# Performance work log

Hardware: AMD Instinct MI355X
Metric: run time of the kernel (lower is better)

Reference implementation:

```python
import jax, jax.numpy as jnp
import numpy as np

B, T, NIV, H = 2048, 64, 10, 128
DT = 0.01


def _uniform(key, shape, fan_in, dtype=jnp.float32):
    bound = 1.0 / np.sqrt(fan_in)
    return jax.random.uniform(key, shape, minval=-bound, maxval=bound, dtype=dtype)


def setup_inputs() -> dict:
    key = jax.random.key(0)
    ks = jax.random.split(key, 12)
    eye = jnp.array([1.0, 0.0, 0.0, 1.0, 0.0, 1.0], dtype=jnp.float32)
    eps = jax.random.normal(ks[0], (B, T, 6), dtype=jnp.float32) * 0.1 + eye
    # free-energy MLP: layers [6+NIV, H, H, 1] (torch Linear init, stored as [in,out])
    wW1 = _uniform(ks[1], (6 + NIV, H), 6 + NIV)
    wb1 = _uniform(ks[2], (H,), 6 + NIV)
    wW2 = _uniform(ks[3], (H, H), H)
    wb2 = _uniform(ks[4], (H,), H)
    wW3 = _uniform(ks[5], (H, 1), H)
    wb3 = _uniform(ks[6], (1,), H)
    # dissipation MLP: layers [NIV, H, H, 1]; last layer is ConvexLayer (weight squared, no bias)
    dW1 = _uniform(ks[7], (NIV, H), NIV)
    db1 = _uniform(ks[8], (H,), NIV)
    dW2 = _uniform(ks[9], (H, H), H)
    db2 = _uniform(ks[10], (H,), H)
    dWc = _uniform(ks[11], (H, 1), H)
    return {"eps": eps, "wW1": wW1, "wb1": wb1, "wW2": wW2, "wb2": wb2,
            "wW3": wW3, "wb3": wb3, "dW1": dW1, "db1": db1, "dW2": dW2,
            "db2": db2, "dWc": dWc}


def reference(eps, wW1, wb1, wW2, wb2, wW3, wb3, dW1, db1, dW2, db2, dWc):
    dtype = eps.dtype
    eye = jnp.array([1.0, 0.0, 0.0, 1.0, 0.0, 1.0], dtype=dtype)
    relu2 = lambda x: jnp.square(jax.nn.relu(x))  # ReLUSquared

    def free_energy(e, xi):
        # e: [B,6], xi: [B,NIV] -> scalar potential per sample [B,1]
        x = jnp.concatenate([e - eye, xi], axis=-1)
        x = relu2(x @ wW1 + wb1)
        x = relu2(x @ wW2 + wb2)
        return x @ wW3 + wb3

    def dissipation(d):
        # d: [B,NIV] -> [B,1]; final ConvexLayer uses squared weights, no bias
        x = relu2(d @ dW1 + db1)
        x = relu2(x @ dW2 + db2)
        return x @ jnp.square(dWc)

    # grad of summed scalar potential == per-sample grads (as in torch.autograd.grad)
    grad_W = jax.grad(lambda e, xi: free_energy(e, xi).sum(), argnums=(0, 1))
    grad_D = jax.grad(lambda d: dissipation(d).sum())

    def step(xi, e_t):
        stress, df = grad_W(e_t, xi)          # dW/deps, dW/dxi
        increment = grad_D(-df)               # dD*/dd evaluated at d = -df
        return xi + DT * increment, stress

    xi0 = jnp.zeros((eps.shape[0], dW1.shape[0]), dtype=dtype)
    _, shat = jax.lax.scan(step, xi0, jnp.swapaxes(eps, 0, 1))  # scan over time
    return jnp.swapaxes(shat, 0, 1)  # [B, T, 6]
```

## Files before the change

### kernel.cpp

```cpp
#include <hip/hip_runtime.h>
#include <hip/hip_bf16.h>


#define NIV 10
#define DT_C 0.01f

__device__ __forceinline__ float bcast(float v, int l) {
    return __int_as_float(__builtin_amdgcn_readlane(__float_as_int(v), l));
}

__global__ __launch_bounds__(512, 2) void cm_kernel(
    const float* __restrict__ eps,
    const float* __restrict__ gwW1, const float* __restrict__ gwb1,
    const float* __restrict__ gwW2, const float* __restrict__ gwb2,
    const float* __restrict__ gwW3,
    const float* __restrict__ gdW1, const float* __restrict__ gdb1,
    const float* __restrict__ gdW2, const float* __restrict__ gdb2,
    const float* __restrict__ gdWc,
    float* __restrict__ out)
{
    __shared__ __align__(16) float sW2[16384];
    __shared__ __align__(16) float sD2[16384];
    __shared__ __align__(16) float sW1[2048];
    __shared__ __align__(16) float sW1T[2048];
    __shared__ __align__(16) float sD1[1280];
    __shared__ __align__(16) float sD1T[1536];
    __shared__ float sb1[128], sb2[128], sW3[128], sdb1[128], sdb2[128], sDc2[128];

    const int tid = threadIdx.x;

    for (int i = tid; i < 16384; i += 512) {
        int r = i >> 7, c = i & 127;
        int idx = (r << 7) + ((((c >> 1) ^ (r >> 1)) & 63) << 1) + (c & 1);
        sW2[idx] = gwW2[i];
        sD2[idx] = gdW2[i];
    }
    for (int i = tid; i < 2048; i += 512) {
        sW1[i] = gwW1[i];
        int k = i >> 7, r = i & 127;
        sW1T[r * 16 + k] = gwW1[i];
    }
    for (int i = tid; i < 1280; i += 512) sD1[i] = gdW1[i];
    for (int i = tid; i < 1536; i += 512) {
        int r = i / 12, m = i - r * 12;
        sD1T[i] = (m < 10) ? gdW1[m * 128 + r] : 0.f;
    }
    if (tid < 128) {
        sb1[tid]  = gwb1[tid];
        sb2[tid]  = gwb2[tid];
        sW3[tid]  = gwW3[tid];
        sdb1[tid] = gdb1[tid];
        sdb2[tid] = gdb2[tid];
        float w = gdWc[tid];
        sDc2[tid] = w * w;
    }
    __syncthreads();

    const int lane = tid & 63;
    const int wv   = tid >> 6;
    const int b    = blockIdx.x * 8 + wv;
    const int c0   = lane * 2, c1 = lane * 2 + 1;
    const int k16  = lane & 15;
    const int k12  = (k16 < 12) ? k16 : 0;

    float xi[NIV];
#pragma unroll
    for (int m = 0; m < NIV; ++m) xi[m] = 0.f;

    const float* ep = eps + b * (64 * 6);
    float*       op = out + b * (64 * 6);

    for (int t = 0; t < 64; ++t) {
        float x0[16];
        x0[0] = ep[t*6+0] - 1.f; x0[1] = ep[t*6+1];       x0[2] = ep[t*6+2];
        x0[3] = ep[t*6+3] - 1.f; x0[4] = ep[t*6+4];       x0[5] = ep[t*6+5] - 1.f;
#pragma unroll
        for (int m = 0; m < NIV; ++m) x0[6+m] = xi[m];

        float z1a = sb1[c0], z1b = sb1[c1];
#pragma unroll
        for (int k = 0; k < 16; ++k) {
            z1a = fmaf(x0[k], sW1[k*128 + c0], z1a);
            z1b = fmaf(x0[k], sW1[k*128 + c1], z1b);
        }
        float r1a = fmaxf(z1a, 0.f), r1b = fmaxf(z1b, 0.f);
        float a1a = r1a * r1a,       a1b = r1b * r1b;

        float z2a = sb2[c0], z2b = sb2[c1];
#pragma unroll 16
        for (int j = 0; j < 64; ++j) {
            float v0 = bcast(a1a, j), v1 = bcast(a1b, j);
            int o = (lane ^ j) << 1;
            const float2 w0 = *(const float2*)(sW2 + (j << 8) + o);
            const float2 w1 = *(const float2*)(sW2 + (j << 8) + 128 + o);
            z2a = fmaf(v0, w0.x, z2a); z2a = fmaf(v1, w1.x, z2a);
            z2b = fmaf(v0, w0.y, z2b); z2b = fmaf(v1, w1.y, z2b);
        }
        float r2a = fmaxf(z2a, 0.f), r2b = fmaxf(z2b, 0.f);
        float gza = 2.f * r2a * sW3[c0], gzb = 2.f * r2b * sW3[c1];

        float g1a = 0.f, g1b = 0.f;
#pragma unroll 16
        for (int j = 0; j < 64; ++j) {
            float v0 = bcast(gza, j), v1 = bcast(gzb, j);
            int o = (lane ^ j) << 1;
            const float2 wa = *(const float2*)(sW2 + c0*128 + o);
            const float2 wb = *(const float2*)(sW2 + c1*128 + o);
            g1a = fmaf(wa.x, v0, g1a); g1a = fmaf(wa.y, v1, g1a);
            g1b = fmaf(wb.x, v0, g1b); g1b = fmaf(wb.y, v1, g1b);
        }
        float gz1a = 2.f * g1a * r1a, gz1b = 2.f * g1b * r1b;

        float gx = 0.f;
#pragma unroll 16
        for (int j = 0; j < 64; ++j) {
            float v0 = bcast(gz1a, j), v1 = bcast(gz1b, j);
            gx = fmaf(v0, sW1T[(j << 5) + k16],      gx);
            gx = fmaf(v1, sW1T[(j << 5) + 16 + k16], gx);
        }
        if (lane < 6) op[t*6 + lane] = gx;

        float dm[NIV];
#pragma unroll
        for (int m = 0; m < NIV; ++m) dm[m] = -bcast(gx, 6 + m);

        float u1a = sdb1[c0], u1b = sdb1[c1];
#pragma unroll
        for (int m = 0; m < NIV; ++m) {
            u1a = fmaf(dm[m], sD1[m*128 + c0], u1a);
            u1b = fmaf(dm[m], sD1[m*128 + c1], u1b);
        }
        float p1a = fmaxf(u1a, 0.f), p1b = fmaxf(u1b, 0.f);
        float q1a = p1a * p1a,       q1b = p1b * p1b;

        float u2a = sdb2[c0], u2b = sdb2[c1];
#pragma unroll 16
        for (int j = 0; j < 64; ++j) {
            float v0 = bcast(q1a, j), v1 = bcast(q1b, j);
            int o = (lane ^ j) << 1;
            const float2 w0 = *(const float2*)(sD2 + (j << 8) + o);
            const float2 w1 = *(const float2*)(sD2 + (j << 8) + 128 + o);
            u2a = fmaf(v0, w0.x, u2a); u2a = fmaf(v1, w1.x, u2a);
            u2b = fmaf(v0, w0.y, u2b); u2b = fmaf(v1, w1.y, u2b);
        }
        float hu2a = 2.f * fmaxf(u2a, 0.f) * sDc2[c0];
        float hu2b = 2.f * fmaxf(u2b, 0.f) * sDc2[c1];

        float h1a = 0.f, h1b = 0.f;
#pragma unroll 16
        for (int j = 0; j < 64; ++j) {
            float v0 = bcast(hu2a, j), v1 = bcast(hu2b, j);
            int o = (lane ^ j) << 1;
            const float2 wa = *(const float2*)(sD2 + c0*128 + o);
            const float2 wb = *(const float2*)(sD2 + c1*128 + o);
            h1a = fmaf(wa.x, v0, h1a); h1a = fmaf(wa.y, v1, h1a);
            h1b = fmaf(wb.x, v0, h1b); h1b = fmaf(wb.y, v1, h1b);
        }
        float hu1a = 2.f * h1a * p1a, hu1b = 2.f * h1b * p1b;

        float gd = 0.f;
#pragma unroll 16
        for (int j = 0; j < 64; ++j) {
            float v0 = bcast(hu1a, j), v1 = bcast(hu1b, j);
            gd = fmaf(v0, sD1T[j*24 + k12],      gd);
            gd = fmaf(v1, sD1T[j*24 + 12 + k12], gd);
        }

#pragma unroll
        for (int m = 0; m < NIV; ++m) xi[m] = fmaf(DT_C, bcast(gd, m), xi[m]);
    }
}

extern "C" void kernel_launch(void* const* d_in, const int* in_sizes, int n_in,
                              void* d_out, int out_size, void* d_ws, size_t ws_size,
                              hipStream_t stream) {
    const float* eps = (const float*)d_in[0];
    const float* wW1 = (const float*)d_in[1];
    const float* wb1 = (const float*)d_in[2];
    const float* wW2 = (const float*)d_in[3];
    const float* wb2 = (const float*)d_in[4];
    const float* wW3 = (const float*)d_in[5];
    const float* dW1 = (const float*)d_in[7];
    const float* db1 = (const float*)d_in[8];
    const float* dW2 = (const float*)d_in[9];
    const float* db2 = (const float*)d_in[10];
    const float* dWc = (const float*)d_in[11];
    float* out = (float*)d_out;

    cm_kernel<<<dim3(256), dim3(512), 0, stream>>>(
        eps, wW1, wb1, wW2, wb2, wW3, dW1, db1, dW2, db2, dWc, out);
}
```

Before: 1.005 ms.

## Rewrite recurrent MLP step on MFMA with split fp16 hi/lo precision

Result: slower. 1.501 ms (+49.4%).

```diff
diff --git a/kernel.cpp b/kernel.cpp
--- a/kernel.cpp
+++ b/kernel.cpp
@@ -2,191 +2,401 @@
 #include <hip/hip_bf16.h>
 
 
-#define NIV 10
+typedef _Float16 h8 __attribute__((ext_vector_type(8)));
+typedef _Float16 h4 __attribute__((ext_vector_type(4)));
+typedef float    f4 __attribute__((ext_vector_type(4)));
+
+#define MFMA16(a,b,c) __builtin_amdgcn_mfma_f32_16x16x32_f16((a),(b),(c),0,0,0)
+#define LBAR() asm volatile("s_waitcnt lgkmcnt(0)" ::: "memory")
 #define DT_C 0.01f
 
-__device__ __forceinline__ float bcast(float v, int l) {
-    return __int_as_float(__builtin_amdgcn_readlane(__float_as_int(v), l));
-}
-
-__global__ __launch_bounds__(512, 2) void cm_kernel(
-    const float* __restrict__ eps,
-    const float* __restrict__ gwW1, const float* __restrict__ gwb1,
-    const float* __restrict__ gwW2, const float* __restrict__ gwb2,
-    const float* __restrict__ gwW3,
-    const float* __restrict__ gdW1, const float* __restrict__ gdb1,
-    const float* __restrict__ gdW2, const float* __restrict__ gdb2,
-    const float* __restrict__ gdWc,
-    float* __restrict__ out)
+#define OFF_W2T 0
+#define OFF_W2  32768
+#define OFF_D2T 65536
+#define OFF_D2  98304
+#define OFF_W1T 131072
+#define OFF_D1T 135168
+#define OFF_W1R 139264
+#define OFF_D1R 143360
+#define OFF_TB  147456
+#define IMG_BYTES 150528
+#define OFF_ACTH 150528
+#define OFF_ACTL 154624
+#define OFF_GBUF 158720
+#define LDS_BYTES 160000
+#define WS_LOBIG 150528
+#define WS_Z1LO  281600
+#define WS_U1LO  289792
+#define WS_GXLO  297984
+#define WS_GDLO  302080
+
+__device__ __forceinline__ int swz8(int c, int r){ return (((c>>3) ^ (r&15))<<3) | (c&7); }
+
+__device__ __forceinline__ float hiPart(float v){
+  float hf = (float)(_Float16)v;
+  if (fabsf(v) < 6.1035156e-5f) hf = 0.f;
+  return hf;
+}
+__device__ __forceinline__ void splitHL(float v, _Float16 &hi, _Float16 &lo){
+  float hf = hiPart(v);
+  hi = (_Float16)hf;
+  lo = (_Float16)((v - hf) * 2048.f);
+}
+
+__global__ void cm_prep(const float* __restrict__ wW1, const float* __restrict__ wb1,
+                        const float* __restrict__ wW2, const float* __restrict__ wb2,
+                        const float* __restrict__ wW3,
+                        const float* __restrict__ dW1, const float* __restrict__ db1,
+                        const float* __restrict__ dW2, const float* __restrict__ db2,
+                        const float* __restrict__ dWc,
+                        unsigned char* __restrict__ ws)
 {
-    __shared__ __align__(16) float sW2[16384];
-    __shared__ __align__(16) float sD2[16384];
-    __shared__ __align__(16) float sW1[2048];
-    __shared__ __align__(16) float sW1T[2048];
-    __shared__ __align__(16) float sD1[1280];
-    __shared__ __align__(16) float sD1T[1536];
-    __shared__ float sb1[128], sb2[128], sW3[128], sdb1[128], sdb2[128], sDc2[128];
-
-    const int tid = threadIdx.x;
-
-    for (int i = tid; i < 16384; i += 512) {
-        int r = i >> 7, c = i & 127;
-        int idx = (r << 7) + ((((c >> 1) ^ (r >> 1)) & 63) << 1) + (c & 1);
-        sW2[idx] = gwW2[i];
-        sD2[idx] = gdW2[i];
-    }
-    for (int i = tid; i < 2048; i += 512) {
-        sW1[i] = gwW1[i];
-        int k = i >> 7, r = i & 127;
-        sW1T[r * 16 + k] = gwW1[i];
-    }
-    for (int i = tid; i < 1280; i += 512) sD1[i] = gdW1[i];
-    for (int i = tid; i < 1536; i += 512) {
-        int r = i / 12, m = i - r * 12;
-        sD1T[i] = (m < 10) ? gdW1[m * 128 + r] : 0.f;
-    }
-    if (tid < 128) {
-        sb1[tid]  = gwb1[tid];
-        sb2[tid]  = gwb2[tid];
-        sW3[tid]  = gwW3[tid];
-        sdb1[tid] = gdb1[tid];
-        sdb2[tid] = gdb2[tid];
-        float w = gdWc[tid];
-        sDc2[tid] = w * w;
-    }
-    __syncthreads();
-
-    const int lane = tid & 63;
-    const int wv   = tid >> 6;
-    const int b    = blockIdx.x * 8 + wv;
-    const int c0   = lane * 2, c1 = lane * 2 + 1;
-    const int k16  = lane & 15;
-    const int k12  = (k16 < 12) ? k16 : 0;
-
-    float xi[NIV];
-#pragma unroll
-    for (int m = 0; m < NIV; ++m) xi[m] = 0.f;
-
-    const float* ep = eps + b * (64 * 6);
-    float*       op = out + b * (64 * 6);
-
-    for (int t = 0; t < 64; ++t) {
-        float x0[16];
-        x0[0] = ep[t*6+0] - 1.f; x0[1] = ep[t*6+1];       x0[2] = ep[t*6+2];
-        x0[3] = ep[t*6+3] - 1.f; x0[4] = ep[t*6+4];       x0[5] = ep[t*6+5] - 1.f;
-#pragma unroll
-        for (int m = 0; m < NIV; ++m) x0[6+m] = xi[m];
-
-        float z1a = sb1[c0], z1b = sb1[c1];
-#pragma unroll
-        for (int k = 0; k < 16; ++k) {
-            z1a = fmaf(x0[k], sW1[k*128 + c0], z1a);
-            z1b = fmaf(x0[k], sW1[k*128 + c1], z1b);
-        }
-        float r1a = fmaxf(z1a, 0.f), r1b = fmaxf(z1b, 0.f);
-        float a1a = r1a * r1a,       a1b = r1b * r1b;
-
-        float z2a = sb2[c0], z2b = sb2[c1];
-#pragma unroll 16
-        for (int j = 0; j < 64; ++j) {
-            float v0 = bcast(a1a, j), v1 = bcast(a1b, j);
-            int o = (lane ^ j) << 1;
-            const float2 w0 = *(const float2*)(sW2 + (j << 8) + o);
-            const float2 w1 = *(const float2*)(sW2 + (j << 8) + 128 + o);
-            z2a = fmaf(v0, w0.x, z2a); z2a = fmaf(v1, w1.x, z2a);
-            z2b = fmaf(v0, w0.y, z2b); z2b = fmaf(v1, w1.y, z2b);
-        }
-        float r2a = fmaxf(z2a, 0.f), r2b = fmaxf(z2b, 0.f);
-        float gza = 2.f * r2a * sW3[c0], gzb = 2.f * r2b * sW3[c1];
-
-        float g1a = 0.f, g1b = 0.f;
-#pragma unroll 16
-        for (int j = 0; j < 64; ++j) {
-            float v0 = bcast(gza, j), v1 = bcast(gzb, j);
-            int o = (lane ^ j) << 1;
-            const float2 wa = *(const float2*)(sW2 + c0*128 + o);
-            const float2 wb = *(const float2*)(sW2 + c1*128 + o);
-            g1a = fmaf(wa.x, v0, g1a); g1a = fmaf(wa.y, v1, g1a);
-            g1b = fmaf(wb.x, v0, g1b); g1b = fmaf(wb.y, v1, g1b);
-        }
-        float gz1a = 2.f * g1a * r1a, gz1b = 2.f * g1b * r1b;
-
-        float gx = 0.f;
-#pragma unroll 16
-        for (int j = 0; j < 64; ++j) {
-            float v0 = bcast(gz1a, j), v1 = bcast(gz1b, j);
-            gx = fmaf(v0, sW1T[(j << 5) + k16],      gx);
-            gx = fmaf(v1, sW1T[(j << 5) + 16 + k16], gx);
-        }
-        if (lane < 6) op[t*6 + lane] = gx;
-
-        float dm[NIV];
-#pragma unroll
-        for (int m = 0; m < NIV; ++m) dm[m] = -bcast(gx, 6 + m);
-
-        float u1a = sdb1[c0], u1b = sdb1[c1];
-#pragma unroll
-        for (int m = 0; m < NIV; ++m) {
-            u1a = fmaf(dm[m], sD1[m*128 + c0], u1a);
-            u1b = fmaf(dm[m], sD1[m*128 + c1], u1b);
-        }
-        float p1a = fmaxf(u1a, 0.f), p1b = fmaxf(u1b, 0.f);
-        float q1a = p1a * p1a,       q1b = p1b * p1b;
-
-        float u2a = sdb2[c0], u2b = sdb2[c1];
-#pragma unroll 16
-        for (int j = 0; j < 64; ++j) {
-            float v0 = bcast(q1a, j), v1 = bcast(q1b, j);
-            int o = (lane ^ j) << 1;
-            const float2 w0 = *(const float2*)(sD2 + (j << 8) + o);
-            const float2 w1 = *(const float2*)(sD2 + (j << 8) + 128 + o);
-            u2a = fmaf(v0, w0.x, u2a); u2a = fmaf(v1, w1.x, u2a);
-            u2b = fmaf(v0, w0.y, u2b); u2b = fmaf(v1, w1.y, u2b);
-        }
-        float hu2a = 2.f * fmaxf(u2a, 0.f) * sDc2[c0];
-        float hu2b = 2.f * fmaxf(u2b, 0.f) * sDc2[c1];
-
-        float h1a = 0.f, h1b = 0.f;
-#pragma unroll 16
-        for (int j = 0; j < 64; ++j) {
-            float v0 = bcast(hu2a, j), v1 = bcast(hu2b, j);
-            int o = (lane ^ j) << 1;
-            const float2 wa = *(const float2*)(sD2 + c0*128 + o);
-            const float2 wb = *(const float2*)(sD2 + c1*128 + o);
-            h1a = fmaf(wa.x, v0, h1a); h1a = fmaf(wa.y, v1, h1a);
-            h1b = fmaf(wb.x, v0, h1b); h1b = fmaf(wb.y, v1, h1b);
-        }
-        float hu1a = 2.f * h1a * p1a, hu1b = 2.f * h1b * p1b;
-
-        float gd = 0.f;
-#pragma unroll 16
-        for (int j = 0; j < 64; ++j) {
-            float v0 = bcast(hu1a, j), v1 = bcast(hu1b, j);
-            gd = fmaf(v0, sD1T[j*24 + k12],      gd);
-            gd = fmaf(v1, sD1T[j*24 + 12 + k12], gd);
-        }
-
-#pragma unroll
-        for (int m = 0; m < NIV; ++m) xi[m] = fmaf(DT_C, bcast(gd, m), xi[m]);
-    }
+  const int tid = blockIdx.x * blockDim.x + threadIdx.x;
+  const int nth = gridDim.x * blockDim.x;
+
+  _Float16* img = (_Float16*)ws;
+  for (int i = tid; i < 65536; i += nth){
+    int arr = i >> 14, e = i & 16383, r = e >> 7, c = e & 127;
+    const float* src = (arr < 2) ? wW2 : dW2;
+    float v = (arr & 1) ? src[r*128 + c] : src[c*128 + r];
+    img[arr*16384 + r*128 + swz8(c, r)] = (_Float16)hiPart(v);
+  }
+  { _Float16* p = (_Float16*)(ws + OFF_W1T);
+    for (int i = tid; i < 2048; i += nth){ int n = i>>4, k = i&15; p[n*16+k] = (_Float16)hiPart(wW1[k*128+n]); } }
+  { _Float16* p = (_Float16*)(ws + OFF_D1T);
+    for (int i = tid; i < 2048; i += nth){ int n = i>>4, m = i&15;
+      float v = (m<10) ? dW1[m*128+n] : 0.f; p[n*16+m] = (_Float16)hiPart(v); } }
+  { _Float16* p = (_Float16*)(ws + OFF_W1R);
+    for (int i = tid; i < 2048; i += nth){ int k = i>>7, c = i&127;
+      p[k*128 + swz8(c,k)] = (_Float16)hiPart(wW1[k*128+c]); } }
+  { _Float16* p = (_Float16*)(ws + OFF_D1R);
+    for (int i = tid; i < 2048; i += nth){ int m = i>>7, c = i&127;
+      float v = (m<10) ? dW1[m*128+c] : 0.f; p[m*128 + swz8(c,m)] = (_Float16)hiPart(v); } }
+  { float* tb = (float*)(ws + OFF_TB);
+    for (int i = tid; i < 128; i += nth){
+      tb[i] = wb1[i]; tb[128+i] = wb2[i]; tb[256+i] = db1[i]; tb[384+i] = db2[i];
+      tb[512+i] = wW3[i]; float w = dWc[i]; tb[640+i] = w*w; } }
+  { _Float16* lob = (_Float16*)(ws + WS_LOBIG);
+    for (int i = tid; i < 65536; i += nth){
+      int j = i&7, lane = (i>>3)&63, kt = (i>>9)&3, rt = (i>>11)&7, arr = i>>14;
+      int row = rt*16 + (lane&15), col = kt*32 + (lane>>4)*8 + j;
+      const float* src = (arr < 2) ? wW2 : dW2;
+      float v = (arr & 1) ? src[row*128 + col] : src[col*128 + row];
+      float hf = hiPart(v);
+      lob[i] = (_Float16)((v - hf)*2048.f);
+    } }
+  { _Float16* p = (_Float16*)(ws + WS_Z1LO);
+    for (int i = tid; i < 4096; i += nth){
+      int j = i&7, lane = (i>>3)&63, ct = i>>9;
+      int row = ct*16 + (lane&15), k = (lane>>4)*8 + j;
+      float v = (k < 16) ? wW1[k*128 + row] : 0.f;
+      float hf = hiPart(v); p[i] = (_Float16)((v-hf)*2048.f); } }
+  { _Float16* p = (_Float16*)(ws + WS_U1LO);
+    for (int i = tid; i < 4096; i += nth){
+      int j = i&7, lane = (i>>3)&63, ct = i>>9;
+      int row = ct*16 + (lane&15), m = (lane>>4)*8 + j;
+      float v = (m < 10) ? dW1[m*128 + row] : 0.f;
+      float hf = hiPart(v); p[i] = (_Float16)((v-hf)*2048.f); } }
+  { _Float16* p = (_Float16*)(ws + WS_GXLO);
+    for (int i = tid; i < 2048; i += nth){
+      int j = i&7, lane = (i>>3)&63, kt = i>>9;
+      int rk = lane&15, col = kt*32 + (lane>>4)*8 + j;
+      float v = wW1[rk*128 + col];
+      float hf = hiPart(v); p[i] = (_Float16)((v-hf)*2048.f); } }
+  { _Float16* p = (_Float16*)(ws + WS_GDLO);
+    for (int i = tid; i < 2048; i += nth){
+      int j = i&7, lane = (i>>3)&63, kt = i>>9;
+      int rm = lane&15, col = kt*32 + (lane>>4)*8 + j;
+      float v = (rm < 10) ? dW1[rm*128 + col] : 0.f;
+      float hf = hiPart(v); p[i] = (_Float16)((v-hf)*2048.f); } }
+}
+
+__device__ __forceinline__ void loadAct(const _Float16* actH, const _Float16* actL,
+                                        h8 (&aH)[4], h8 (&aL)[4], int ln15, int g){
+#pragma unroll
+  for (int kt = 0; kt < 4; ++kt){
+    int idx = ln15*128 + ((((kt*4+g) ^ ln15)) << 3);
+    aH[kt] = *(const h8*)&actH[idx];
+    aL[kt] = *(const h8*)&actL[idx];
+  }
+}
+
+__device__ __forceinline__ void packTile(f4 v, int ct, _Float16* actH, _Float16* actL, int ln15, int g){
+  h4 hh, ll;
+#pragma unroll
+  for (int r = 0; r < 4; ++r){ _Float16 a, b; splitHL(v[r], a, b); hh[r] = a; ll[r] = b; }
+  int idx = ln15*128 + ((((ct*2 + (g>>1)) ^ ln15)) << 3) + ((g&1) << 2);
+  *(h4*)&actH[idx] = hh;
+  *(h4*)&actL[idx] = ll;
+}
+
+__device__ __forceinline__ void bigLayer(const _Float16* Whi, const h8* Wlo, const float* bias,
+                                         const h8 (&aH)[4], const h8 (&aL)[4], f4 (&cc)[8],
+                                         int ln15, int g, int lane){
+#pragma unroll
+  for (int ct = 0; ct < 8; ++ct){
+    f4 c0;
+    if (bias) c0 = *(const f4*)&bias[ct*16 + g*4];
+    else      c0 = (f4){0.f,0.f,0.f,0.f};
+    f4 c1 = {0.f,0.f,0.f,0.f};
+#pragma unroll
+    for (int kt = 0; kt < 4; ++kt){
+      h8 wh = *(const h8*)&Whi[(ct*16 + ln15)*128 + ((((kt*4+g) ^ ln15)) << 3)];
+      h8 wl = Wlo[(ct*4 + kt)*64 + lane];
+      c0 = MFMA16(wh, aH[kt], c0);
+      c1 = MFMA16(wh, aL[kt], c1);
+      c1 = MFMA16(wl, aH[kt], c1);
+    }
+    cc[ct] = c0 + c1 * (1.f/2048.f);
+  }
+}
+
+__device__ __forceinline__ void smallLayer(const _Float16* Whi, const h8* Wlo, const float* bias,
+                                           h8 bH, h8 bL, f4 (&cc)[8], int ln15, int g, int lane){
+#pragma unroll
+  for (int ct = 0; ct < 8; ++ct){
+    f4 c0 = *(const f4*)&bias[ct*16 + g*4];
+    f4 c1 = {0.f,0.f,0.f,0.f};
+    h8 wh = *(const h8*)&Whi[(ct*16 + ln15)*16 + ((g&1) << 3)];
+    h8 wl = Wlo[ct*64 + lane];
+    c0 = MFMA16(wh, bH, c0);
+    c1 = MFMA16(wh, bL, c1);
+    c1 = MFMA16(wl, bH, c1);
+    cc[ct] = c0 + c1 * (1.f/2048.f);
+  }
+}
+
+__device__ __forceinline__ f4 gradLayer16(const _Float16* Whi, const h8* Wlo,
+                                          const h8 (&aH)[4], const h8 (&aL)[4],
+                                          int ln15, int g, int lane){
+  f4 c0 = {0.f,0.f,0.f,0.f}, c1 = {0.f,0.f,0.f,0.f};
+#pragma unroll
+  for (int kt = 0; kt < 4; ++kt){
+    h8 wh = *(const h8*)&Whi[ln15*128 + ((((kt*4+g) ^ ln15)) << 3)];
+    h8 wl = Wlo[kt*64 + lane];
+    c0 = MFMA16(wh, aH[kt], c0);
+    c1 = MFMA16(wh, aL[kt], c1);
+    c1 = MFMA16(wl, aH[kt], c1);
+  }
+  return c0 + c1 * (1.f/2048.f);
+}
+
+__global__ __launch_bounds__(64, 1) void cm_mfma(const float* __restrict__ eps,
+                                                 const unsigned char* __restrict__ ws,
+                                                 float* __restrict__ out)
+{
+  __shared__ __align__(16) unsigned char LDS[LDS_BYTES];
+  const int lane = threadIdx.x;
+  const int ln15 = lane & 15, g = lane >> 4;
+
+  {
+    const f4* src = (const f4*)ws;
+    f4* dst = (f4*)LDS;
+    for (int i = lane; i < IMG_BYTES/16; i += 64) dst[i] = src[i];
+  }
+  asm volatile("s_waitcnt vmcnt(0) lgkmcnt(0)" ::: "memory");
+
+  const _Float16* W2T = (const _Float16*)(LDS + OFF_W2T);
+  const _Float16* W2R = (const _Float16*)(LDS + OFF_W2);
+  const _Float16* D2T = (const _Float16*)(LDS + OFF_D2T);
+  const _Float16* D2R = (const _Float16*)(LDS + OFF_D2);
+  const _Float16* W1T = (const _Float16*)(LDS + OFF_W1T);
+  const _Float16* D1T = (const _Float16*)(LDS + OFF_D1T);
+  const _Float16* W1R = (const _Float16*)(LDS + OFF_W1R);
+  const _Float16* D1R = (const _Float16*)(LDS + OFF_D1R);
+  const float*    tb  = (const float*)(LDS + OFF_TB);
+  _Float16* actH = (_Float16*)(LDS + OFF_ACTH);
+  _Float16* actL = (_Float16*)(LDS + OFF_ACTL);
+  float*    gbuf = (float*)(LDS + OFF_GBUF);
+
+  const h8* loW2T = (const h8*)(ws + WS_LOBIG);
+  const h8* loW2R = (const h8*)(ws + WS_LOBIG + 32768);
+  const h8* loD2T = (const h8*)(ws + WS_LOBIG + 65536);
+  const h8* loD2R = (const h8*)(ws + WS_LOBIG + 98304);
+  const h8* loZ1  = (const h8*)(ws + WS_Z1LO);
+  const h8* loU1  = (const h8*)(ws + WS_U1LO);
+  const h8* loGX  = (const h8*)(ws + WS_GXLO);
+  const h8* loGD  = (const h8*)(ws + WS_GDLO);
+
+  const int b0 = blockIdx.x * 16;
+  const float* ep = eps + (size_t)(b0 + ln15) * 384;
+  float*       op = out + (size_t)(b0 + ln15) * 384;
+
+  float xiS[8];
+#pragma unroll
+  for (int j = 0; j < 8; ++j) xiS[j] = 0.f;
+
+  float e0=0,e1=0,e2=0,e3=0,e4=0,e5=0;
+  if (g == 0){
+    float2 a = *(const float2*)(ep);     e0=a.x; e1=a.y;
+    float2 b = *(const float2*)(ep + 2); e2=b.x; e3=b.y;
+    float2 c = *(const float2*)(ep + 4); e4=c.x; e5=c.y;
+  }
+
+  for (int t = 0; t < 64; ++t){
+    float xv[8];
+    if (g == 0){
+      xv[0]=e0-1.f; xv[1]=e1; xv[2]=e2; xv[3]=e3-1.f; xv[4]=e4; xv[5]=e5-1.f;
+      xv[6]=xiS[0]; xv[7]=xiS[1];
+    } else if (g == 1){
+#pragma unroll
+      for (int j = 0; j < 8; ++j) xv[j] = xiS[j];
+    } else {
+#pragma unroll
+      for (int j = 0; j < 8; ++j) xv[j] = 0.f;
+    }
+    h8 xHi, xLo;
+#pragma unroll
+    for (int j = 0; j < 8; ++j){ _Float16 a, b; splitHL(xv[j], a, b); xHi[j]=a; xLo[j]=b; }
+
+    float n0=e0,n1=e1,n2=e2,n3=e3,n4=e4,n5=e5;
+    if (g == 0 && t < 63){
+      const float* p = ep + (t+1)*6;
+      float2 a = *(const float2*)(p);     n0=a.x; n1=a.y;
+      float2 b = *(const float2*)(p + 2); n2=b.x; n3=b.y;
+      float2 c = *(const float2*)(p + 4); n4=c.x; n5=c.y;
+    }
+
+    f4 cc[8], r1v[8], p1v[8];
+    h8 aH[4], aL[4];
+
+    smallLayer(W1T, loZ1, tb + 0, xHi, xLo, cc, ln15, g, lane);
+#pragma unroll
+    for (int ct = 0; ct < 8; ++ct){
+      f4 r, a;
+#pragma unroll
+      for (int q = 0; q < 4; ++q){ float rr = fmaxf(cc[ct][q], 0.f); r[q] = rr; a[q] = rr*rr; }
+      r1v[ct] = r;
+      packTile(a, ct, actH, actL, ln15, g);
+    }
+    LBAR();
+
+    loadAct(actH, actL, aH, aL, ln15, g);
+    bigLayer(W2T, loW2T, tb + 128, aH, aL, cc, ln15, g, lane);
+#pragma unroll
+    for (int ct = 0; ct < 8; ++ct){
+      f4 w3 = *(const f4*)&tb[512 + ct*16 + g*4];
+      f4 gz;
+#pragma unroll
+      for (int q = 0; q < 4; ++q) gz[q] = 2.f * fmaxf(cc[ct][q], 0.f) * w3[q];
+      packTile(gz, ct, actH, actL, ln15, g);
+    }
+    LBAR();
+
+    loadAct(actH, actL, aH, aL, ln15, g);
+    bigLayer(W2R, loW2R, nullptr, aH, aL, cc, ln15, g, lane);
+#pragma unroll
+    for (int ct = 0; ct < 8; ++ct){
+      f4 gz;
+#pragma unroll
+      for (int q = 0; q < 4; ++q) gz[q] = 2.f * cc[ct][q] * r1v[ct][q];
+      packTile(gz, ct, actH, actL, ln15, g);
+    }
+    LBAR();
+
+    loadAct(actH, actL, aH, aL, ln15, g);
+    f4 gx = gradLayer16(W1R, loGX, aH, aL, ln15, g, lane);
+    if (g == 0){
+      *(float2*)(op + t*6)     = make_float2(gx[0], gx[1]);
+      *(float2*)(op + t*6 + 2) = make_float2(gx[2], gx[3]);
+    } else if (g == 1){
+      *(float2*)(op + t*6 + 4) = make_float2(gx[0], gx[1]);
+    }
+    *(f4*)(gbuf + ln15*20 + g*4) = gx;
+    LBAR();
+
+    float dv[8];
+    if (g == 0){
+      float2 a = *(const float2*)(gbuf + ln15*20 + 6);
+      f4     b = *(const f4*)    (gbuf + ln15*20 + 8);
+      float2 c = *(const float2*)(gbuf + ln15*20 + 12);
+      dv[0]=-a.x; dv[1]=-a.y; dv[2]=-b[0]; dv[3]=-b[1]; dv[4]=-b[2]; dv[5]=-b[3]; dv[6]=-c.x; dv[7]=-c.y;
+    } else if (g == 1){
+      float2 a = *(const float2*)(gbuf + ln15*20 + 14);
+      dv[0]=-a.x; dv[1]=-a.y;
+#pragma unroll
+      for (int j = 2; j < 8; ++j) dv[j] = 0.f;
+    } else {
+#pragma unroll
+      for (int j = 0; j < 8; ++j) dv[j] = 0.f;
+    }
+    h8 dHi, dLo;
+#pragma unroll
+    for (int j = 0; j < 8; ++j){ _Float16 a, b; splitHL(dv[j], a, b); dHi[j]=a; dLo[j]=b; }
+
+    smallLayer(D1T, loU1, tb + 256, dHi, dLo, cc, ln15, g, lane);
+#pragma unroll
+    for (int ct = 0; ct < 8; ++ct){
+      f4 r, a;
+#pragma unroll
+      for (int q = 0; q < 4; ++q){ float rr = fmaxf(cc[ct][q], 0.f); r[q] = rr; a[q] = rr*rr; }
+      p1v[ct] = r;
+      packTile(a, ct, actH, actL, ln15, g);
+    }
+    LBAR();
+
+    loadAct(actH, actL, aH, aL, ln15, g);
+    bigLayer(D2T, loD2T, tb + 384, aH, aL, cc, ln15, g, lane);
+#pragma unroll
+    for (int ct = 0; ct < 8; ++ct){
+      f4 dc = *(const f4*)&tb[640 + ct*16 + g*4];
+      f4 hu;
+#pragma unroll
+      for (int q = 0; q < 4; ++q) hu[q] = 2.f * fmaxf(cc[ct][q], 0.f) * dc[q];
+      packTile(hu, ct, actH, actL, ln15, g);
+    }
+    LBAR();
+
+    loadAct(actH, actL, aH, aL, ln15, g);
+    bigLayer(D2R, loD2R, nullptr, aH, aL, cc, ln15, g, lane);
+#pragma unroll
+    for (int ct = 0; ct < 8; ++ct){
+      f4 hu;
+#pragma unroll
+      for (int q = 0; q < 4; ++q) hu[q] = 2.f * cc[ct][q] * p1v[ct][q];
+      packTile(hu, ct, actH, actL, ln15, g);
+    }
+    LBAR();
+
+    loadAct(actH, actL, aH, aL, ln15, g);
+    f4 gd = gradLayer16(D1R, loGD, aH, aL, ln15, g, lane);
+    *(f4*)(gbuf + ln15*20 + g*4) = gd;
+    LBAR();
+
+    if (g == 0){
+      float2 a = *(const float2*)(gbuf + ln15*20);
+      xiS[0] += DT_C * a.x; xiS[1] += DT_C * a.y;
+    } else if (g == 1){
+      float2 a = *(const float2*)(gbuf + ln15*20 + 2);
+      f4     b = *(const f4*)    (gbuf + ln15*20 + 4);
+      float2 c = *(const float2*)(gbuf + ln15*20 + 8);
+      xiS[0] += DT_C * a.x; xiS[1] += DT_C * a.y;
+      xiS[2] += DT_C * b[0]; xiS[3] += DT_C * b[1]; xiS[4] += DT_C * b[2]; xiS[5] += DT_C * b[3];
+      xiS[6] += DT_C * c.x; xiS[7] += DT_C * c.y;
+    }
+
+    e0=n0; e1=n1; e2=n2; e3=n3; e4=n4; e5=n5;
+  }
 }
 
 extern "C" void kernel_launch(void* const* d_in, const int* in_sizes, int n_in,
                               void* d_out, int out_size, void* d_ws, size_t ws_size,
                               hipStream_t stream) {
-    const float* eps = (const float*)d_in[0];
-    const float* wW1 = (const float*)d_in[1];
-    const float* wb1 = (const float*)d_in[2];
-    const float* wW2 = (const float*)d_in[3];
-    const float* wb2 = (const float*)d_in[4];
-    const float* wW3 = (const float*)d_in[5];
-    const float* dW1 = (const float*)d_in[7];
-    const float* db1 = (const float*)d_in[8];
-    const float* dW2 = (const float*)d_in[9];
-    const float* db2 = (const float*)d_in[10];
-    const float* dWc = (const float*)d_in[11];
-    float* out = (float*)d_out;
-
-    cm_kernel<<<dim3(256), dim3(512), 0, stream>>>(
-        eps, wW1, wb1, wW2, wb2, wW3, dW1, db1, dW2, db2, dWc, out);
-}
+  const float* eps = (const float*)d_in[0];
+  const float* wW1 = (const float*)d_in[1];
+  const float* wb1 = (const float*)d_in[2];
+  const float* wW2 = (const float*)d_in[3];
+  const float* wb2 = (const float*)d_in[4];
+  const float* wW3 = (const float*)d_in[5];
+  const float* dW1 = (const float*)d_in[7];
+  const float* db1 = (const float*)d_in[8];
+  const float* dW2 = (const float*)d_in[9];
+  const float* db2 = (const float*)d_in[10];
+  const float* dWc = (const float*)d_in[11];
+  unsigned char* ws = (unsigned char*)d_ws;
+  float* out = (float*)d_out;
+
+  cm_prep<<<dim3(256), dim3(256), 0, stream>>>(wW1, wb1, wW2, wb2, wW3,
+                                               dW1, db1, dW2, db2, dWc, ws);
+  cm_mfma<<<dim3(128), dim3(64), 0, stream>>>(eps, ws, out);
+}
```
